# Kernel optimization log

Measured on AMD Instinct MI355X. Metric: run time of the kernel, lower is better.

The kernel has to match this reference:

```python
import jax, jax.numpy as jnp
import numpy as np

N_NODES = 100_000
N_EDGES = 1_600_000
F_IN = 128
NHID = 128
G = 64            # num graphs in the batch
N_CLASSES = 2
EMB = NHID * 6    # embedding_data dim so concat dim == NHID*8


def _lin_init(k, fi, fo):
    s = 1.0 / np.sqrt(fi)
    k1, k2 = jax.random.split(k)
    w = jax.random.uniform(k1, (fi, fo), jnp.float32, -s, s)
    b = jax.random.uniform(k2, (fo,), jnp.float32, -s, s)
    return w, b


def setup_inputs() -> dict:
    key = jax.random.key(0)
    ks = jax.random.split(key, 12)
    x = jax.random.normal(ks[0], (N_NODES, F_IN), jnp.float32)
    edge_index = jax.random.randint(ks[1], (2, N_EDGES), 0, N_NODES, dtype=jnp.int32)
    per = N_NODES // G
    batch = jnp.minimum(jnp.arange(N_NODES, dtype=jnp.int32) // per, G - 1)  # sorted, even split
    embedding_data = jax.random.normal(ks[2], (G, EMB), jnp.float32)
    conv_w, conv_b = _lin_init(ks[3], F_IN, NHID)
    lin0_w, lin0_b = _lin_init(ks[4], F_IN, NHID)
    lin1_w, lin1_b = _lin_init(ks[5], NHID * 8, NHID * 4)
    lin2_w, lin2_b = _lin_init(ks[6], NHID * 4, NHID * 2)
    lin3_w, lin3_b = _lin_init(ks[7], NHID * 2, NHID)
    lin4_w, lin4_b = _lin_init(ks[8], NHID, N_CLASSES)
    return {
        "x": x, "embedding_data": embedding_data,
        "conv_w": conv_w, "conv_b": conv_b,
        "lin0_w": lin0_w, "lin0_b": lin0_b,
        "lin1_w": lin1_w, "lin1_b": lin1_b,
        "lin2_w": lin2_w, "lin2_b": lin2_b,
        "lin3_w": lin3_w, "lin3_b": lin3_b,
        "lin4_w": lin4_w, "lin4_b": lin4_b,
        "edge_index": edge_index, "batch": batch,
    }


def _gcn_conv(x, edge_index, w, b):
    """PyG GCNConv: add self-loops, symmetric deg^-1/2 normalization, linear, scatter-add."""
    n = x.shape[0]
    loop = jnp.arange(n, dtype=edge_index.dtype)
    src = jnp.concatenate([edge_index[0], loop])
    dst = jnp.concatenate([edge_index[1], loop])
    deg = jax.ops.segment_sum(jnp.ones_like(dst, dtype=x.dtype), dst, num_segments=n)
    dinv = jnp.where(deg > 0, jax.lax.rsqrt(deg), 0.0)
    norm = dinv[src] * dinv[dst]                     # [E+N]
    h = x @ w                                        # [N, NHID]
    msg = h[src] * norm[:, None]                     # gather  [E+N, NHID]
    out = jax.ops.segment_sum(msg, dst, num_segments=n)  # scatter-add
    return out + b


def reference(x, embedding_data, conv_w, conv_b, lin0_w, lin0_b,
              lin1_w, lin1_b, lin2_w, lin2_b, lin3_w, lin3_b,
              lin4_w, lin4_b, edge_index, batch):
    h = jax.nn.relu(_gcn_conv(x, edge_index, conv_w, conv_b))   # [N, NHID]
    pooled = jax.ops.segment_max(h, batch, num_segments=G)      # global max pool [G, NHID]
    # first node of each graph (batch is sorted)
    first_idx = jnp.searchsorted(batch, jnp.arange(G, dtype=batch.dtype))
    news = jax.nn.relu(x[first_idx] @ lin0_w + lin0_b)          # [G, NHID]
    z = jnp.concatenate([pooled, news, embedding_data], axis=1) # [G, NHID*8]
    z = jnp.tanh(z @ lin1_w + lin1_b)   # dropout = identity (eval mode)
    z = jnp.tanh(z @ lin2_w + lin2_b)
    z = jnp.tanh(z @ lin3_w + lin3_b)
    return jax.nn.log_softmax(z @ lin4_w + lin4_b, axis=-1)     # [G, N_CLASSES]
```

## Files before the change

kernel.cpp:

```cpp
#include <hip/hip_runtime.h>
#include <hip/hip_bf16.h>

#define N_NODES 100000
#define N_EDGES 1600000
#define F 128
#define G 64
#define EMB 768
#define PER 1562
#define CAP 96
#define NBUCK 256
#define BNODES 391
#define BCAP 7680
#define TILE 8192
#define NBIN 196
#define GEMM_GRID 512

typedef __hip_bfloat16 bf16;
typedef __attribute__((ext_vector_type(8))) short short8;
typedef __attribute__((ext_vector_type(4))) float f32x4;
typedef unsigned long long u64;

__device__ __forceinline__ float b2f(bf16 v) { return __bfloat162float(v); }
__device__ __forceinline__ short f2bs(float v) {
    bf16 b = __float2bfloat16(v);
    return *reinterpret_cast<short*>(&b);
}

__global__ void k_init(float* __restrict__ pooled, int* __restrict__ gcur) {
    int i = blockIdx.x * 256 + threadIdx.x;
    if (i < G * F) pooled[i] = 0.0f;
    if (i < NBUCK) gcur[i] = 0;
}

__global__ __launch_bounds__(256) void k_fat(const int* __restrict__ ei,
                                             int* __restrict__ gcur,
                                             u64* __restrict__ stage,
                                             const float* __restrict__ x,
                                             const float* __restrict__ w,
                                             bf16* __restrict__ h) {
    int t = threadIdx.x;
    if (blockIdx.x < NBIN) {
        __shared__ int hist[NBUCK];
        __shared__ int gbase[NBUCK];
        __shared__ int offs[NBUCK];
        hist[t] = 0; offs[t] = 0;
        __syncthreads();
        int e0 = blockIdx.x * TILE;
        int e1 = min(e0 + TILE, N_EDGES);
        for (int e = e0 + t; e < e1; e += 256)
            atomicAdd(&hist[ei[N_EDGES + e] / BNODES], 1);
        __syncthreads();
        gbase[t] = atomicAdd(&gcur[t], hist[t]);
        __syncthreads();
        for (int e = e0 + t; e < e1; e += 256) {
            int src = ei[e];
            int dst = ei[N_EDGES + e];
            int b = dst / BNODES;
            int pos = gbase[b] + atomicAdd(&offs[b], 1);
            stage[(size_t)b * BCAP + pos] =
                (u64)(unsigned)src | ((u64)(unsigned)dst << 32);
        }
    } else {
        __shared__ short wfrag[16384];
        for (int i = t; i < 16384; i += 256) {
            int j    = i & 7;
            int lane = (i >> 3) & 63;
            int kb   = (i >> 9) & 3;
            int ct   = i >> 11;
            int k    = kb * 32 + (lane >> 4) * 8 + j;
            int n    = ct * 16 + (lane & 15);
            wfrag[i] = f2bs(w[k * 128 + n]);
        }
        __syncthreads();

        int wv = t >> 6, lane = t & 63;
        int m = lane & 15, q = lane >> 4;
        int nchunks = (N_NODES + 63) / 64;
        for (int chunk = blockIdx.x - NBIN; chunk < nchunks; chunk += GEMM_GRID) {
            int row = chunk * 64 + wv * 16 + m;
            int rr = (row < N_NODES) ? row : 0;
            short8 a[4];
#pragma unroll
            for (int kb = 0; kb < 4; ++kb) {
                const float* src = x + (size_t)rr * F + kb * 32 + q * 8;
                float4 v0 = *(const float4*)src;
                float4 v1 = *(const float4*)(src + 4);
                short8 av;
                av[0] = f2bs(v0.x); av[1] = f2bs(v0.y); av[2] = f2bs(v0.z); av[3] = f2bs(v0.w);
                av[4] = f2bs(v1.x); av[5] = f2bs(v1.y); av[6] = f2bs(v1.z); av[7] = f2bs(v1.w);
                a[kb] = av;
            }
            f32x4 acc[8];
#pragma unroll
            for (int ct = 0; ct < 8; ++ct) {
                f32x4 c = {0.f, 0.f, 0.f, 0.f};
#pragma unroll
                for (int kb = 0; kb < 4; ++kb) {
                    short8 bfr = *(const short8*)&wfrag[((ct * 4 + kb) * 64 + lane) * 8];
                    c = __builtin_amdgcn_mfma_f32_16x16x32_bf16(a[kb], bfr, c, 0, 0, 0);
                }
                acc[ct] = c;
            }
            int rbase = chunk * 64 + wv * 16 + q * 4;
#pragma unroll
            for (int ct = 0; ct < 8; ++ct)
#pragma unroll
                for (int r = 0; r < 4; ++r) {
                    int ro = rbase + r;
                    if (ro < N_NODES) h[(size_t)ro * F + ct * 16 + m] = __float2bfloat16(acc[ct][r]);
                }
        }
    }
}

__global__ __launch_bounds__(1024) void k_scat(const u64* __restrict__ stage,
                                               const int* __restrict__ gcur,
                                               int* __restrict__ cursor,
                                               float* __restrict__ dinv,
                                               int* __restrict__ slots) {
    __shared__ int lcur[BNODES];
    int b = blockIdx.x;
    int t = threadIdx.x;
    int nbase = b * BNODES;
    int bn = min(BNODES, N_NODES - nbase);
    if (bn <= 0) return;
    for (int l = t; l < bn; l += 1024) lcur[l] = 0;
    __syncthreads();
    int cnt = min(gcur[b], BCAP);
    const u64* sp = stage + (size_t)b * BCAP;
    for (int i = t; i < cnt; i += 1024) {
        u64 p = sp[i];
        int src = (int)(p & 0xffffffffu);
        int dst = (int)(p >> 32);
        int pos = atomicAdd(&lcur[dst - nbase], 1);
        if (pos < CAP) slots[(size_t)dst * CAP + pos] = src;
    }
    __syncthreads();
    for (int l = t; l < bn; l += 1024) {
        int c = lcur[l];
        cursor[nbase + l] = c;
        dinv[nbase + l] = rsqrtf((float)(c + 1));
    }
}

__global__ __launch_bounds__(256) void k_agg(const bf16* __restrict__ h,
                                             const float* __restrict__ dinv,
                                             const int* __restrict__ slots,
                                             const int* __restrict__ cnt,
                                             const float* __restrict__ cb,
                                             float* __restrict__ pooled) {
    int wv = threadIdx.x >> 6;
    int lane = threadIdx.x & 63;
    int nb = blockIdx.x * 16 + wv * 4;
    int c[4];
    const int* sl[4];
    float a0[4] = {0.f, 0.f, 0.f, 0.f};
    float a1[4] = {0.f, 0.f, 0.f, 0.f};
    int cmax = 0;
#pragma unroll
    for (int u = 0; u < 4; ++u) {
        c[u] = min(cnt[nb + u], CAP);
        cmax = max(cmax, c[u]);
        sl[u] = slots + (size_t)(nb + u) * CAP;
    }
    for (int base = 0; base < cmax; base += 64) {
        int idx[4];
        float dsv[4];
        int nlmax = 0;
#pragma unroll
        for (int u = 0; u < 4; ++u) {
            int nl = min(64, c[u] - base);
            nlmax = max(nlmax, nl);
            idx[u] = 0; dsv[u] = 0.f;
            if (lane < nl) { idx[u] = sl[u][base + lane]; dsv[u] = dinv[idx[u]]; }
        }
        for (int j = 0; j < 64; j += 4) {
            if (j >= nlmax) break;
            int s[16];
            float ww[16];
#pragma unroll
            for (int uu = 0; uu < 4; ++uu)
#pragma unroll
                for (int u = 0; u < 4; ++u) {
                    s[uu * 4 + u] = __shfl(idx[u], j + uu);
                    ww[uu * 4 + u] = __shfl(dsv[u], j + uu);
                }
            __hip_bfloat162 hv[16];
#pragma unroll
            for (int i = 0; i < 16; ++i)
                hv[i] = *(const __hip_bfloat162*)&h[(size_t)s[i] * F + 2 * lane];
#pragma unroll
            for (int uu = 0; uu < 4; ++uu)
#pragma unroll
                for (int u = 0; u < 4; ++u) {
                    float wgt = ww[uu * 4 + u];
                    a0[u] += b2f(hv[uu * 4 + u].x) * wgt;
                    a1[u] += b2f(hv[uu * 4 + u].y) * wgt;
                }
        }
    }
    float cb0 = cb[2 * lane], cb1 = cb[2 * lane + 1];
    float s0[4], s1[4];
#pragma unroll
    for (int u = 0; u < 4; ++u) {
        float dn = dinv[nb + u];
        __hip_bfloat162 hn = *(const __hip_bfloat162*)&h[(size_t)(nb + u) * F + 2 * lane];
        s0[u] = fmaxf(a0[u] * dn + b2f(hn.x) * dn * dn + cb0, 0.f);
        s1[u] = fmaxf(a1[u] * dn + b2f(hn.y) * dn * dn + cb1, 0.f);
    }

    __shared__ float red[16][128];
    int n0 = blockIdx.x * 16;
    int g0 = min(n0 / PER, G - 1);
    int gL = min((n0 + 15) / PER, G - 1);
    if (g0 == gL) {
#pragma unroll
        for (int u = 0; u < 4; ++u) {
            red[wv * 4 + u][2 * lane] = s0[u];
            red[wv * 4 + u][2 * lane + 1] = s1[u];
        }
        __syncthreads();
        if (wv == 0) {
            float m0 = red[0][2 * lane], m1 = red[0][2 * lane + 1];
#pragma unroll
            for (int r = 1; r < 16; ++r) {
                m0 = fmaxf(m0, red[r][2 * lane]);
                m1 = fmaxf(m1, red[r][2 * lane + 1]);
            }
            atomicMax((int*)&pooled[g0 * F + 2 * lane],     __float_as_int(m0));
            atomicMax((int*)&pooled[g0 * F + 2 * lane + 1], __float_as_int(m1));
        }
    } else {
#pragma unroll
        for (int u = 0; u < 4; ++u) {
            int g = min((nb + u) / PER, G - 1);
            atomicMax((int*)&pooled[g * F + 2 * lane],     __float_as_int(s0[u]));
            atomicMax((int*)&pooled[g * F + 2 * lane + 1], __float_as_int(s1[u]));
        }
    }
}

__global__ __launch_bounds__(256) void k_l1(const float* __restrict__ x,
                                            const float* __restrict__ pooled,
                                            const float* __restrict__ emb,
                                            const float* __restrict__ l0w,
                                            const float* __restrict__ l0b,
                                            const float* __restrict__ w1,
                                            const float* __restrict__ b1,
                                            float* __restrict__ z1) {
    int g = blockIdx.x >> 3, jc = blockIdx.x & 7;
    int t = threadIdx.x;
    __shared__ float zs[1024];
    __shared__ float xs[128];
    __shared__ float psum[4][64];
    if (t < 128) {
        xs[t] = x[(size_t)(g * PER) * F + t];
        zs[t] = pooled[g * 128 + t];
    }
    for (int i = t; i < EMB; i += 256) zs[256 + i] = emb[g * EMB + i];
    __syncthreads();
    if (t < 128) {
        float acc = l0b[t];
        for (int k = 0; k < 128; ++k) acc += xs[k] * l0w[k * 128 + t];
        zs[128 + t] = fmaxf(acc, 0.f);
    }
    __syncthreads();
    int j = t & 63, kc = t >> 6;
    float acc = 0.f;
    const float* wp = w1 + (size_t)(kc * 256) * 512 + jc * 64 + j;
#pragma unroll 4
    for (int k = 0; k < 256; ++k)
        acc += zs[kc * 256 + k] * wp[(size_t)k * 512];
    psum[kc][j] = acc;
    __syncthreads();
    if (t < 64) {
        float s = b1[jc * 64 + t] + psum[0][t] + psum[1][t] + psum[2][t] + psum[3][t];
        z1[g * 512 + jc * 64 + t] = tanhf(s);
    }
}

__global__ __launch_bounds__(256) void k_l2(const float* __restrict__ z1,
                                            const float* __restrict__ w2,
                                            const float* __restrict__ b2,
                                            float* __restrict__ z2) {
    int g = blockIdx.x >> 2, jc = blockIdx.x & 3;
    int t = threadIdx.x, j = t & 63, kc = t >> 6;
    __shared__ float zs[512];
    __shared__ float psum[4][64];
    for (int i = t; i < 512; i += 256) zs[i] = z1[g * 512 + i];
    __syncthreads();
    float acc = 0.f;
    const float* wp = w2 + (size_t)(kc * 128) * 256 + jc * 64 + j;
#pragma unroll 4
    for (int k = 0; k < 128; ++k)
        acc += zs[kc * 128 + k] * wp[(size_t)k * 256];
    psum[kc][j] = acc;
    __syncthreads();
    if (t < 64) {
        float s = b2[jc * 64 + t] + psum[0][t] + psum[1][t] + psum[2][t] + psum[3][t];
        z2[g * 256 + jc * 64 + t] = tanhf(s);
    }
}

__global__ __launch_bounds__(256) void k_l3out(const float* __restrict__ z2,
                                               const float* __restrict__ w3,
                                               const float* __restrict__ b3,
                                               const float* __restrict__ w4,
                                               const float* __restrict__ b4,
                                               float* __restrict__ out) {
    int g = blockIdx.x, t = threadIdx.x;
    __shared__ float zs[256];
    __shared__ float psum[2][128];
    __shared__ float z3s[128];
    zs[t] = z2[g * 256 + t];
    __syncthreads();
    int j = t & 127, kc = t >> 7;
    float acc = 0.f;
    const float* wp = w3 + (size_t)(kc * 128) * 128 + j;
#pragma unroll 4
    for (int k = 0; k < 128; ++k)
        acc += zs[kc * 128 + k] * wp[(size_t)k * 128];
    psum[kc][j] = acc;
    __syncthreads();
    if (t < 128) z3s[t] = tanhf(b3[t] + psum[0][t] + psum[1][t]);
    __syncthreads();
    if (t < 2) {
        float l = b4[t];
        for (int k = 0; k < 128; ++k) l += z3s[k] * w4[k * 2 + t];
        psum[0][t] = l;
    }
    __syncthreads();
    if (t == 0) {
        float l0 = psum[0][0], l1 = psum[0][1];
        float m = fmaxf(l0, l1);
        float lse = m + logf(expf(l0 - m) + expf(l1 - m));
        out[g * 2 + 0] = l0 - lse;
        out[g * 2 + 1] = l1 - lse;
    }
}

extern "C" void kernel_launch(void* const* d_in, const int* in_sizes, int n_in,
                              void* d_out, int out_size, void* d_ws, size_t ws_size,
                              hipStream_t stream) {
    const float* x      = (const float*)d_in[0];
    const float* emb    = (const float*)d_in[1];
    const float* conv_w = (const float*)d_in[2];
    const float* conv_b = (const float*)d_in[3];
    const float* lin0_w = (const float*)d_in[4];
    const float* lin0_b = (const float*)d_in[5];
    const float* lin1_w = (const float*)d_in[6];
    const float* lin1_b = (const float*)d_in[7];
    const float* lin2_w = (const float*)d_in[8];
    const float* lin2_b = (const float*)d_in[9];
    const float* lin3_w = (const float*)d_in[10];
    const float* lin3_b = (const float*)d_in[11];
    const float* lin4_w = (const float*)d_in[12];
    const float* lin4_b = (const float*)d_in[13];
    const int*   ei     = (const int*)d_in[14];
    float* out = (float*)d_out;

    char* ws = (char*)d_ws;
    int*   cursor = (int*)ws;                         ws += (size_t)N_NODES * 4;
    float* dinv   = (float*)ws;                       ws += (size_t)N_NODES * 4;
    int*   slots  = (int*)ws;                         ws += (size_t)N_NODES * CAP * 4;
    bf16*  h      = (bf16*)ws;                        ws += (size_t)N_NODES * F * 2;
    float* pooled = (float*)ws;                       ws += (size_t)G * F * 4;
    int*   gcur   = (int*)ws;                         ws += (size_t)NBUCK * 4;
    u64*   stage  = (u64*)ws;                         ws += (size_t)NBUCK * BCAP * 8;
    float* z1     = (float*)ws;                       ws += (size_t)G * 512 * 4;
    float* z2     = (float*)ws;                       ws += (size_t)G * 256 * 4;

    k_init<<<(G * F + 255) / 256, 256, 0, stream>>>(pooled, gcur);
    k_fat<<<NBIN + GEMM_GRID, 256, 0, stream>>>(ei, gcur, stage, x, conv_w, h);
    k_scat<<<NBUCK, 1024, 0, stream>>>(stage, gcur, cursor, dinv, slots);
    k_agg<<<N_NODES / 16, 256, 0, stream>>>(h, dinv, slots, cursor, conv_b, pooled);
    k_l1<<<G * 8, 256, 0, stream>>>(x, pooled, emb, lin0_w, lin0_b, lin1_w, lin1_b, z1);
    k_l2<<<G * 4, 256, 0, stream>>>(z1, lin2_w, lin2_b, z2);
    k_l3out<<<G, 256, 0, stream>>>(z2, lin3_w, lin3_b, lin4_w, lin4_b, out);
}
```

Measured before the change: 308.7 us.

## Pack staged edges into 32 bits, fuse tail MLP kernels, replace init kernel with memset

Staged edge records shrink from 64-bit (src,dst) pairs to 32-bit words holding src in 17 bits and the bucket-local dst above it, halving staging traffic in the binning and scatter kernels. The binning tile is halved so twice as many blocks bin edges in parallel. The lin2 and lin3/output kernels merge into one per-graph kernel, which drops a launch and the z2 round trip but runs lin2 with only 64 blocks. The init kernel becomes a hipMemsetAsync over the adjacent pooled and bucket-counter buffers.

```diff
diff --git a/kernel.cpp b/kernel.cpp
--- a/kernel.cpp
+++ b/kernel.cpp
@@ -11,14 +11,14 @@
 #define NBUCK 256
 #define BNODES 391
 #define BCAP 7680
-#define TILE 8192
-#define NBIN 196
+#define TILE 4096
+#define NBIN 391
 #define GEMM_GRID 512
 
 typedef __hip_bfloat16 bf16;
 typedef __attribute__((ext_vector_type(8))) short short8;
 typedef __attribute__((ext_vector_type(4))) float f32x4;
-typedef unsigned long long u64;
+typedef unsigned int u32;
 
 __device__ __forceinline__ float b2f(bf16 v) { return __bfloat162float(v); }
 __device__ __forceinline__ short f2bs(float v) {
@@ -26,15 +26,9 @@
     return *reinterpret_cast<short*>(&b);
 }
 
-__global__ void k_init(float* __restrict__ pooled, int* __restrict__ gcur) {
-    int i = blockIdx.x * 256 + threadIdx.x;
-    if (i < G * F) pooled[i] = 0.0f;
-    if (i < NBUCK) gcur[i] = 0;
-}
-
 __global__ __launch_bounds__(256) void k_fat(const int* __restrict__ ei,
                                              int* __restrict__ gcur,
-                                             u64* __restrict__ stage,
+                                             u32* __restrict__ stage,
                                              const float* __restrict__ x,
                                              const float* __restrict__ w,
                                              bf16* __restrict__ h) {
@@ -56,9 +50,9 @@
             int src = ei[e];
             int dst = ei[N_EDGES + e];
             int b = dst / BNODES;
+            int dl = dst - b * BNODES;
             int pos = gbase[b] + atomicAdd(&offs[b], 1);
-            stage[(size_t)b * BCAP + pos] =
-                (u64)(unsigned)src | ((u64)(unsigned)dst << 32);
+            stage[(size_t)b * BCAP + pos] = (u32)src | ((u32)dl << 17);
         }
     } else {
         __shared__ short wfrag[16384];
@@ -113,7 +107,7 @@
     }
 }
 
-__global__ __launch_bounds__(1024) void k_scat(const u64* __restrict__ stage,
+__global__ __launch_bounds__(1024) void k_scat(const u32* __restrict__ stage,
                                                const int* __restrict__ gcur,
                                                int* __restrict__ cursor,
                                                float* __restrict__ dinv,
@@ -127,13 +121,13 @@
     for (int l = t; l < bn; l += 1024) lcur[l] = 0;
     __syncthreads();
     int cnt = min(gcur[b], BCAP);
-    const u64* sp = stage + (size_t)b * BCAP;
+    const u32* sp = stage + (size_t)b * BCAP;
     for (int i = t; i < cnt; i += 1024) {
-        u64 p = sp[i];
-        int src = (int)(p & 0xffffffffu);
-        int dst = (int)(p >> 32);
-        int pos = atomicAdd(&lcur[dst - nbase], 1);
-        if (pos < CAP) slots[(size_t)dst * CAP + pos] = src;
+        u32 p = sp[i];
+        int src = (int)(p & 0x1FFFFu);
+        int dl  = (int)(p >> 17);
+        int pos = atomicAdd(&lcur[dl], 1);
+        if (pos < CAP) slots[(size_t)(nbase + dl) * CAP + pos] = src;
     }
     __syncthreads();
     for (int l = t; l < bn; l += 1024) {
@@ -279,48 +273,38 @@
     }
 }
 
-__global__ __launch_bounds__(256) void k_l2(const float* __restrict__ z1,
-                                            const float* __restrict__ w2,
-                                            const float* __restrict__ b2,
-                                            float* __restrict__ z2) {
-    int g = blockIdx.x >> 2, jc = blockIdx.x & 3;
-    int t = threadIdx.x, j = t & 63, kc = t >> 6;
+__global__ __launch_bounds__(256) void k_l23out(const float* __restrict__ z1,
+                                                const float* __restrict__ w2,
+                                                const float* __restrict__ b2,
+                                                const float* __restrict__ w3,
+                                                const float* __restrict__ b3,
+                                                const float* __restrict__ w4,
+                                                const float* __restrict__ b4,
+                                                float* __restrict__ out) {
+    int g = blockIdx.x, t = threadIdx.x;
     __shared__ float zs[512];
-    __shared__ float psum[4][64];
-    for (int i = t; i < 512; i += 256) zs[i] = z1[g * 512 + i];
-    __syncthreads();
-    float acc = 0.f;
-    const float* wp = w2 + (size_t)(kc * 128) * 256 + jc * 64 + j;
-#pragma unroll 4
-    for (int k = 0; k < 128; ++k)
-        acc += zs[kc * 128 + k] * wp[(size_t)k * 256];
-    psum[kc][j] = acc;
-    __syncthreads();
-    if (t < 64) {
-        float s = b2[jc * 64 + t] + psum[0][t] + psum[1][t] + psum[2][t] + psum[3][t];
-        z2[g * 256 + jc * 64 + t] = tanhf(s);
-    }
-}
-
-__global__ __launch_bounds__(256) void k_l3out(const float* __restrict__ z2,
-                                               const float* __restrict__ w3,
-                                               const float* __restrict__ b3,
-                                               const float* __restrict__ w4,
-                                               const float* __restrict__ b4,
-                                               float* __restrict__ out) {
-    int g = blockIdx.x, t = threadIdx.x;
-    __shared__ float zs[256];
+    __shared__ float z2s[256];
     __shared__ float psum[2][128];
     __shared__ float z3s[128];
-    zs[t] = z2[g * 256 + t];
-    __syncthreads();
-    int j = t & 127, kc = t >> 7;
-    float acc = 0.f;
-    const float* wp = w3 + (size_t)(kc * 128) * 128 + j;
+    for (int i = t; i < 512; i += 256) zs[i] = z1[g * 512 + i];
+    __syncthreads();
+    {
+        float acc = b2[t];
+        const float* wp = w2 + t;
 #pragma unroll 4
-    for (int k = 0; k < 128; ++k)
-        acc += zs[kc * 128 + k] * wp[(size_t)k * 128];
-    psum[kc][j] = acc;
+        for (int k = 0; k < 512; ++k) acc += zs[k] * wp[(size_t)k * 256];
+        z2s[t] = tanhf(acc);
+    }
+    __syncthreads();
+    {
+        int j = t & 127, kc = t >> 7;
+        float acc = 0.f;
+        const float* wp = w3 + (size_t)(kc * 128) * 128 + j;
+#pragma unroll 4
+        for (int k = 0; k < 128; ++k)
+            acc += z2s[kc * 128 + k] * wp[(size_t)k * 128];
+        psum[kc][j] = acc;
+    }
     __syncthreads();
     if (t < 128) z3s[t] = tanhf(b3[t] + psum[0][t] + psum[1][t]);
     __syncthreads();
@@ -366,15 +350,14 @@
     bf16*  h      = (bf16*)ws;                        ws += (size_t)N_NODES * F * 2;
     float* pooled = (float*)ws;                       ws += (size_t)G * F * 4;
     int*   gcur   = (int*)ws;                         ws += (size_t)NBUCK * 4;
-    u64*   stage  = (u64*)ws;                         ws += (size_t)NBUCK * BCAP * 8;
+    u32*   stage  = (u32*)ws;                         ws += (size_t)NBUCK * BCAP * 4;
     float* z1     = (float*)ws;                       ws += (size_t)G * 512 * 4;
-    float* z2     = (float*)ws;                       ws += (size_t)G * 256 * 4;
-
-    k_init<<<(G * F + 255) / 256, 256, 0, stream>>>(pooled, gcur);
+
+    hipMemsetAsync(pooled, 0, (size_t)G * F * 4 + (size_t)NBUCK * 4, stream);
     k_fat<<<NBIN + GEMM_GRID, 256, 0, stream>>>(ei, gcur, stage, x, conv_w, h);
     k_scat<<<NBUCK, 1024, 0, stream>>>(stage, gcur, cursor, dinv, slots);
     k_agg<<<N_NODES / 16, 256, 0, stream>>>(h, dinv, slots, cursor, conv_b, pooled);
     k_l1<<<G * 8, 256, 0, stream>>>(x, pooled, emb, lin0_w, lin0_b, lin1_w, lin1_b, z1);
-    k_l2<<<G * 4, 256, 0, stream>>>(z1, lin2_w, lin2_b, z2);
-    k_l3out<<<G, 256, 0, stream>>>(z2, lin3_w, lin3_b, lin4_w, lin4_b, out);
-}
+    k_l23out<<<G, 256, 0, stream>>>(z1, lin2_w, lin2_b, lin3_w, lin3_b,
+                                    lin4_w, lin4_b, out);
+}
```

Result: slower. 347.5 us (+12.6%).
